# Optimization experiments

Hardware: AMD Instinct MI355X
Metric: run time of the kernel (lower is better)

The kernel has to match this reference:

```python
import jax, jax.numpy as jnp
import numpy as np

D_MODEL = 1024
NUM_HEADS = 16
D_K = D_MODEL // NUM_HEADS


def setup_inputs() -> dict:
    key = jax.random.key(0)
    ks = jax.random.split(key, 12)
    B, S = 2, 2048
    s = 1.0 / np.sqrt(D_MODEL)
    inp = {
        "query": jax.random.normal(ks[0], (B, S, D_MODEL), jnp.float32),
        "key": jax.random.normal(ks[1], (B, S, D_MODEL), jnp.float32),
        "value": jax.random.normal(ks[2], (B, S, D_MODEL), jnp.float32),
        "Wq": jax.random.normal(ks[3], (D_MODEL, D_MODEL), jnp.float32) * s,
        "bq": jax.random.normal(ks[4], (D_MODEL,), jnp.float32) * s,
        "Wk": jax.random.normal(ks[5], (D_MODEL, D_MODEL), jnp.float32) * s,
        "bk": jax.random.normal(ks[6], (D_MODEL,), jnp.float32) * s,
        "Wv": jax.random.normal(ks[7], (D_MODEL, D_MODEL), jnp.float32) * s,
        "bv": jax.random.normal(ks[8], (D_MODEL,), jnp.float32) * s,
        "Wo": jax.random.normal(ks[9], (D_MODEL, D_MODEL), jnp.float32) * s,
        "bo": jax.random.normal(ks[10], (D_MODEL,), jnp.float32) * s,
    }
    return inp


def _split_heads(x):
    B, S, _ = x.shape
    return x.reshape(B, S, NUM_HEADS, D_K).transpose(0, 2, 1, 3)  # [B,H,S,Dk]


def reference(query, key, value, Wq, bq, Wk, bk, Wv, bv, Wo, bo):
    # Linear projections (torch Linear: x @ W.T + b)
    Q = _split_heads(query @ Wq.T + bq)
    K = _split_heads(key @ Wk.T + bk)
    V = _split_heads(value @ Wv.T + bv)
    scale = 1.0 / jnp.sqrt(jnp.asarray(D_K, Q.dtype))
    scores = jnp.einsum('bhqd,bhkd->bhqk', Q, K) * scale  # [B,H,S,S]
    attn = jax.nn.softmax(scores, axis=-1)
    # dropout is identity in eval mode
    x = jnp.einsum('bhqk,bhkd->bhqd', attn, V)
    B, H, S, Dk = x.shape
    x = x.transpose(0, 2, 1, 3).reshape(B, S, H * Dk)
    return x @ Wo.T + bo
```

## Files before the change

### kernel.cpp

```cpp
#include <hip/hip_runtime.h>
#include <hip/hip_bf16.h>

typedef __bf16 bf16;
typedef __attribute__((ext_vector_type(4))) __bf16 bf16x4;
typedef __attribute__((ext_vector_type(8))) __bf16 bf16x8;
typedef __attribute__((ext_vector_type(4))) float f32x4;
typedef __attribute__((ext_vector_type(16))) float f32x16;
typedef unsigned int u32;

#define D_MODEL 1024
#define NHEADS 16
#define DK 64
#define BATCH 2
#define SEQ 2048
#define NTOK (BATCH * SEQ)

#define QSCALE 0.18033688011112042f

__device__ __forceinline__ u32 cvtpk_bf16(float lo, float hi) {
  u32 r;
  asm("v_cvt_pk_bf16_f32 %0, %1, %2" : "=v"(r) : "v"(lo), "v"(hi));
  return r;
}
__device__ __forceinline__ void plswap(u32& a, u32& b) {
  asm("v_permlane32_swap_b32 %0, %1" : "+v"(a), "+v"(b));
}
__device__ __forceinline__ float fast_exp2(float x) {
#if __has_builtin(__builtin_amdgcn_exp2f)
  return __builtin_amdgcn_exp2f(x);
#else
  return exp2f(x);
#endif
}
__device__ __forceinline__ float xhalf_add(float x) {
  return x + __shfl_xor(x, 32);
}

__device__ __forceinline__ int frag_off_q(int s, int d) {
  return ((s >> 5) << 11) + ((d >> 4) << 9) + ((((d >> 3) & 1) * 32 + (s & 31)) << 3) + (d & 7);
}
__device__ __forceinline__ int frag_off_k(int s, int d) {
  return ((s >> 6) << 12) + ((((s >> 5) & 1) * 4 + (d >> 4)) << 9) +
         ((((d >> 3) & 1) * 32 + (s & 31)) << 3) + (d & 7);
}
__device__ __forceinline__ int frag_off_v(int s, int d) {
  return ((s >> 6) << 12) + (((d >> 5) * 4 + ((s >> 4) & 3)) << 9) +
         ((((s >> 3) & 1) * 32 + (d & 31)) << 3) + (s & 7);
}

__global__ __launch_bounds__(256) void cvt3_kernel(
    const float* __restrict__ s0, const float* __restrict__ s1, const float* __restrict__ s2,
    bf16* __restrict__ d0, bf16* __restrict__ d1, bf16* __restrict__ d2, int n4) {
  int i = blockIdx.x * blockDim.x + threadIdx.x;
  if (i >= n4) return;
  const float* s = blockIdx.y == 0 ? s0 : blockIdx.y == 1 ? s1 : s2;
  bf16* d = blockIdx.y == 0 ? d0 : blockIdx.y == 1 ? d1 : d2;
  float4 v = reinterpret_cast<const float4*>(s)[i];
  bf16x4 o;
  o[0] = (bf16)v.x; o[1] = (bf16)v.y; o[2] = (bf16)v.z; o[3] = (bf16)v.w;
  reinterpret_cast<bf16x4*>(d)[i] = o;
}

__global__ __launch_bounds__(256) void cvt4_kernel(
    const float* __restrict__ s0, const float* __restrict__ s1,
    const float* __restrict__ s2, const float* __restrict__ s3,
    bf16* __restrict__ d0, bf16* __restrict__ d1, bf16* __restrict__ d2, bf16* __restrict__ d3,
    int n4) {
  int i = blockIdx.x * blockDim.x + threadIdx.x;
  if (i >= n4) return;
  const float* s = blockIdx.y == 0 ? s0 : blockIdx.y == 1 ? s1 : blockIdx.y == 2 ? s2 : s3;
  bf16* d = blockIdx.y == 0 ? d0 : blockIdx.y == 1 ? d1 : blockIdx.y == 2 ? d2 : d3;
  float4 v = reinterpret_cast<const float4*>(s)[i];
  bf16x4 o;
  o[0] = (bf16)v.x; o[1] = (bf16)v.y; o[2] = (bf16)v.z; o[3] = (bf16)v.w;
  reinterpret_cast<bf16x4*>(d)[i] = o;
}

#define ASYNC_COPY16(gptr, lptr)                                                \
  __builtin_amdgcn_global_load_lds(                                             \
      (__attribute__((address_space(1))) void*)(gptr),                          \
      (__attribute__((address_space(3))) void*)(lptr), 16, 0, 0)

#define BK 32
#define NSTEP (D_MODEL / BK)

struct ProjArgs {
  const bf16* A[3];
  const bf16* W[3];
  const float* bias[3];
  bf16* out[3];
};

__global__ __launch_bounds__(256) void gemm_proj(ProjArgs pa, int K) {
  __shared__ bf16 smem[2][2][128][BK];
  const int z = blockIdx.z;
  const bf16* A = pa.A[z];
  const bf16* Bw = pa.W[z];
  const int m0 = blockIdx.x * 128;
  const int n0 = blockIdx.y * 128;

  const int t = threadIdx.x;
  const int wave = t >> 6;
  const int lane = t & 63;
  const int wr = (wave >> 1) * 64;
  const int wc = (wave & 1) * 64;
  const int r4 = lane >> 2;
  const int c8 = (lane & 3) * 8;
  const int fr = lane & 15;
  const int fk = (lane >> 4) * 8;

  f32x4 acc[4][4] = {};

#define STAGE_PROJ(buf, kk0)                                                    \
  {                                                                             \
    ASYNC_COPY16(&A[(size_t)(m0 + wave * 16 + r4) * K + (kk0) + c8],            \
                 &smem[buf][0][wave * 16][0]);                                  \
    ASYNC_COPY16(&A[(size_t)(m0 + 64 + wave * 16 + r4) * K + (kk0) + c8],       \
                 &smem[buf][0][64 + wave * 16][0]);                             \
    ASYNC_COPY16(&Bw[(size_t)(n0 + wave * 16 + r4) * K + (kk0) + c8],           \
                 &smem[buf][1][wave * 16][0]);                                  \
    ASYNC_COPY16(&Bw[(size_t)(n0 + 64 + wave * 16 + r4) * K + (kk0) + c8],      \
                 &smem[buf][1][64 + wave * 16][0]);                             \
  }

  STAGE_PROJ(0, 0)
  __syncthreads();

  int cur = 0;
  for (int s = 0; s < NSTEP; s++) {
    if (s + 1 < NSTEP) STAGE_PROJ(cur ^ 1, (s + 1) * BK)

    bf16x8 af[4], bfr[4];
#pragma unroll
    for (int m = 0; m < 4; m++)
      af[m] = *reinterpret_cast<const bf16x8*>(&smem[cur][0][wr + m * 16 + fr][fk]);
#pragma unroll
    for (int n = 0; n < 4; n++)
      bfr[n] = *reinterpret_cast<const bf16x8*>(&smem[cur][1][wc + n * 16 + fr][fk]);
#pragma unroll
    for (int m = 0; m < 4; m++)
#pragma unroll
      for (int n = 0; n < 4; n++)
        acc[m][n] = __builtin_amdgcn_mfma_f32_16x16x32_bf16(af[m], bfr[n], acc[m][n], 0, 0, 0);

    __syncthreads();
    cur ^= 1;
  }

  bf16* cbuf = &smem[0][0][0][0];
  const float scale = (z == 0) ? QSCALE : 1.0f;
  const float* bias = pa.bias[z];
#pragma unroll
  for (int m = 0; m < 4; m++) {
#pragma unroll
    for (int n = 0; n < 4; n++) {
      const int col = n0 + wc + n * 16 + fr;
      const float bv = bias[col];
      const int d = col & (DK - 1);
      const int h_loc = (col >> 6) & 1;
#pragma unroll
      for (int j = 0; j < 4; j++) {
        const int rl = wr + m * 16 + (lane >> 4) * 4 + j;
        const float v = (acc[m][n][j] + bv) * scale;
        int inner;
        if (z == 0)      inner = frag_off_q(rl, d);
        else if (z == 1) inner = frag_off_k(rl, d);
        else             inner = frag_off_v(rl, d);
        cbuf[h_loc * 8192 + inner] = (bf16)v;
      }
    }
  }
  __syncthreads();

  {
    const int bblk = m0 >> 11;
    const int ms = m0 & (SEQ - 1);
    const int h_loc = t >> 7;
    const int tl = t & 127;
    const int h = (n0 >> 6) + h_loc;
    bf16* outp = pa.out[z] + ((size_t)(bblk * NHEADS + h)) * SEQ * DK + (size_t)ms * 64;
#pragma unroll
    for (int c = 0; c < 8; c++) {
      const int off_e = (tl + c * 128) * 8;
      *reinterpret_cast<bf16x8*>(&outp[off_e]) =
          *reinterpret_cast<const bf16x8*>(&cbuf[h_loc * 8192 + off_e]);
    }
  }
}

__global__ __launch_bounds__(256) void gemm_out(
    const bf16* __restrict__ A, const bf16* __restrict__ Bw,
    const float* __restrict__ bias, float* __restrict__ out, int K) {
  __shared__ bf16 AsO[2][128][BK];
  __shared__ bf16 BsO[2][64][BK];
  const int m0 = blockIdx.x * 128;
  const int n0 = blockIdx.y * 64;

  const int t = threadIdx.x;
  const int wave = t >> 6;
  const int lane = t & 63;
  const int wr = (wave >> 1) * 64;
  const int wc = (wave & 1) * 32;
  const int r4 = lane >> 2;
  const int c8 = (lane & 3) * 8;
  const int fr = lane & 15;
  const int fk = (lane >> 4) * 8;

  f32x4 acc[4][2] = {};

#define STAGE_OUT(buf, kk0)                                                     \
  {                                                                             \
    ASYNC_COPY16(&A[(size_t)(m0 + wave * 16 + r4) * K + (kk0) + c8],            \
                 &AsO[buf][wave * 16][0]);                                      \
    ASYNC_COPY16(&A[(size_t)(m0 + 64 + wave * 16 + r4) * K + (kk0) + c8],       \
                 &AsO[buf][64 + wave * 16][0]);                                 \
    ASYNC_COPY16(&Bw[(size_t)(n0 + wave * 16 + r4) * K + (kk0) + c8],           \
                 &BsO[buf][wave * 16][0]);                                      \
  }

  STAGE_OUT(0, 0)
  __syncthreads();

  int cur = 0;
  for (int s = 0; s < NSTEP; s++) {
    if (s + 1 < NSTEP) STAGE_OUT(cur ^ 1, (s + 1) * BK)

    bf16x8 af[4], bfr[2];
#pragma unroll
    for (int m = 0; m < 4; m++)
      af[m] = *reinterpret_cast<const bf16x8*>(&AsO[cur][wr + m * 16 + fr][fk]);
#pragma unroll
    for (int n = 0; n < 2; n++)
      bfr[n] = *reinterpret_cast<const bf16x8*>(&BsO[cur][wc + n * 16 + fr][fk]);
#pragma unroll
    for (int m = 0; m < 4; m++)
#pragma unroll
      for (int n = 0; n < 2; n++)
        acc[m][n] = __builtin_amdgcn_mfma_f32_16x16x32_bf16(af[m], bfr[n], acc[m][n], 0, 0, 0);

    __syncthreads();
    cur ^= 1;
  }

#pragma unroll
  for (int m = 0; m < 4; m++) {
#pragma unroll
    for (int n = 0; n < 2; n++) {
      const int col = n0 + wc + n * 16 + fr;
      const float bv = bias[col];
#pragma unroll
      for (int j = 0; j < 4; j++) {
        const int row = m0 + wr + m * 16 + (lane >> 4) * 4 + j;
        out[(size_t)row * D_MODEL + col] = acc[m][n][j] + bv;
      }
    }
  }
}

#define QBLK 32
#define KVBLK 32
#define NT (SEQ / KVBLK)

__global__ __launch_bounds__(256, 2) void attn_kernel(
    const bf16* __restrict__ Qf,
    const bf16* __restrict__ Kf,
    const bf16* __restrict__ Vf,
    bf16* __restrict__ X) {
  const int lane = threadIdx.x & 63;
  const int wave = threadIdx.x >> 6;

  const int i = blockIdx.x;
  const int xcd = i & 7;
  const int slot = i >> 3;
  const int hgrp = slot >> 4;
  const int xq = slot & 15;
  const int bh = xcd + 8 * hgrp;
  const int bb = bh >> 4, hh = bh & (NHEADS - 1);
  const int q0 = xq * (QBLK * 4) + wave * QBLK;
  const int row = lane & 31, hi = lane >> 5;

  const bf16* Qp = Qf + (size_t)bh * SEQ * DK + (size_t)q0 * DK;
  const bf16* Kp = Kf + (size_t)bh * SEQ * DK;
  const bf16* Vp = Vf + (size_t)bh * SEQ * DK;

  bf16x8 qf[4];
#pragma unroll
  for (int kd = 0; kd < 4; kd++)
    qf[kd] = *reinterpret_cast<const bf16x8*>(&Qp[kd * 512 + lane * 8]);

  f32x16 ot0, ot1, fz;
#pragma unroll
  for (int r = 0; r < 16; r++) { ot0[r] = 0.f; ot1[r] = 0.f; fz[r] = 0.f; }
  float l_run = 0.f;

  bf16x8 ka[4], kb[4];

#define LOADK32(dst, tt)                                                        \
  {                                                                             \
    const bf16* kbase_ = Kp + (size_t)(tt) * 2048 + lane * 8;                   \
    _Pragma("unroll") for (int kd = 0; kd < 4; kd++)                            \
        dst[kd] = *reinterpret_cast<const bf16x8*>(&kbase_[kd * 512]);          \
  }

  LOADK32(ka, 0)
  LOADK32(kb, 1)
  f32x16 sa, sb;
  __builtin_amdgcn_s_setprio(1);
  sa = __builtin_amdgcn_mfma_f32_32x32x16_bf16(ka[0], qf[0], fz, 0, 0, 0);
#pragma unroll
  for (int kd = 1; kd < 4; kd++)
    sa = __builtin_amdgcn_mfma_f32_32x32x16_bf16(ka[kd], qf[kd], sa, 0, 0, 0);
  __builtin_amdgcn_s_setprio(0);

  auto pipe = [&](f32x16& SC, f32x16& SN, bf16x8 (&KN)[4], bf16x8 (&KL)[4], int tc) {
    __builtin_amdgcn_s_setprio(1);
    SN = __builtin_amdgcn_mfma_f32_32x32x16_bf16(KN[0], qf[0], fz, 0, 0, 0);
#pragma unroll
    for (int kd = 1; kd < 4; kd++)
      SN = __builtin_amdgcn_mfma_f32_32x32x16_bf16(KN[kd], qf[kd], SN, 0, 0, 0);
    __builtin_amdgcn_s_setprio(0);

    LOADK32(KL, (tc + 2) & (NT - 1))

    bf16x8 vf[2][2];
    {
      const bf16* vbase_ = Vp + (size_t)(tc >> 1) * 4096 + lane * 8;
      const int so = (tc & 1) * 2;
#pragma unroll
      for (int dh = 0; dh < 2; dh++)
#pragma unroll
        for (int ks = 0; ks < 2; ks++)
          vf[dh][ks] = *reinterpret_cast<const bf16x8*>(
              &vbase_[(dh * 4 + so + ks) * 512]);
    }

    float p[16];
#pragma unroll
    for (int r = 0; r < 16; r++) p[r] = fast_exp2(SC[r]);
    float a8[8];
#pragma unroll
    for (int r = 0; r < 8; r++) a8[r] = p[r] + p[r + 8];
#pragma unroll
    for (int r = 0; r < 4; r++) a8[r] += a8[r + 4];
    l_run += (a8[0] + a8[1]) + (a8[2] + a8[3]);

    u32 c[8];
#pragma unroll
    for (int i2 = 0; i2 < 8; i2++) c[i2] = cvtpk_bf16(p[2 * i2], p[2 * i2 + 1]);
    plswap(c[0], c[2]);   plswap(c[1], c[3]);
    plswap(c[4], c[6]);   plswap(c[5], c[7]);
    bf16x8 pbv[2];
#pragma unroll
    for (int ks = 0; ks < 2; ks++) {
      union { u32 u[4]; bf16x8 v; } pk;
      pk.u[0] = c[ks * 4 + 0]; pk.u[1] = c[ks * 4 + 1];
      pk.u[2] = c[ks * 4 + 2]; pk.u[3] = c[ks * 4 + 3];
      pbv[ks] = pk.v;
    }

    __builtin_amdgcn_s_setprio(1);
    ot0 = __builtin_amdgcn_mfma_f32_32x32x16_bf16(vf[0][0], pbv[0], ot0, 0, 0, 0);
    ot0 = __builtin_amdgcn_mfma_f32_32x32x16_bf16(vf[0][1], pbv[1], ot0, 0, 0, 0);
    ot1 = __builtin_amdgcn_mfma_f32_32x32x16_bf16(vf[1][0], pbv[0], ot1, 0, 0, 0);
    ot1 = __builtin_amdgcn_mfma_f32_32x32x16_bf16(vf[1][1], pbv[1], ot1, 0, 0, 0);
    __builtin_amdgcn_s_setprio(0);
  };

  for (int t = 0; t < NT; t += 2) {
    pipe(sa, sb, kb, ka, t);
    pipe(sb, sa, ka, kb, t + 1);
  }

  l_run = xhalf_add(l_run);

  const float inv = 1.0f / l_run;
  bf16* Xp = X + ((size_t)bb * SEQ + q0 + row) * D_MODEL + hh * DK;
#pragma unroll
  for (int g = 0; g < 4; g++) {
    bf16x4 w0, w1;
#pragma unroll
    for (int j = 0; j < 4; j++) {
      w0[j] = (bf16)(ot0[g * 4 + j] * inv);
      w1[j] = (bf16)(ot1[g * 4 + j] * inv);
    }
    *reinterpret_cast<bf16x4*>(&Xp[g * 8 + hi * 4]) = w0;
    *reinterpret_cast<bf16x4*>(&Xp[32 + g * 8 + hi * 4]) = w1;
  }
}

extern "C" void kernel_launch(void* const* d_in, const int* in_sizes, int n_in,
                              void* d_out, int out_size, void* d_ws, size_t ws_size,
                              hipStream_t stream) {
  const float* q  = (const float*)d_in[0];
  const float* k  = (const float*)d_in[1];
  const float* v  = (const float*)d_in[2];
  const float* Wq = (const float*)d_in[3];
  const float* bq = (const float*)d_in[4];
  const float* Wk = (const float*)d_in[5];
  const float* bk = (const float*)d_in[6];
  const float* Wv = (const float*)d_in[7];
  const float* bv = (const float*)d_in[8];
  const float* Wo = (const float*)d_in[9];
  const float* bo = (const float*)d_in[10];

  char* ws = (char*)d_ws;
  size_t off = 0;
  auto alloc = [&](size_t bytes) -> void* {
    void* p = ws + off;
    off += (bytes + 255) & ~(size_t)255;
    return p;
  };
  const size_t ACT = (size_t)NTOK * D_MODEL;
  const size_t WEL = (size_t)D_MODEL * D_MODEL;

  bf16* Xq  = (bf16*)alloc(ACT * 2);
  bf16* Xk  = (bf16*)alloc(ACT * 2);
  bf16* Xv  = (bf16*)alloc(ACT * 2);
  bf16* Wqb = (bf16*)alloc(WEL * 2);
  bf16* Wkb = (bf16*)alloc(WEL * 2);
  bf16* Wvb = (bf16*)alloc(WEL * 2);
  bf16* Wob = (bf16*)alloc(WEL * 2);
  bf16* Qfb = (bf16*)alloc(ACT * 2);
  bf16* Kfb = (bf16*)alloc(ACT * 2);
  bf16* Vfb = (bf16*)alloc(ACT * 2);
  bf16* Xa  = (bf16*)alloc(ACT * 2);

  {
    int n4 = (int)(ACT / 4);
    cvt3_kernel<<<dim3((n4 + 255) / 256, 3), dim3(256), 0, stream>>>(q, k, v, Xq, Xk, Xv, n4);
  }
  {
    int n4 = (int)(WEL / 4);
    cvt4_kernel<<<dim3((n4 + 255) / 256, 4), dim3(256), 0, stream>>>(
        Wq, Wk, Wv, Wo, Wqb, Wkb, Wvb, Wob, n4);
  }

  ProjArgs pa;
  pa.A[0] = Xq;  pa.A[1] = Xk;  pa.A[2] = Xv;
  pa.W[0] = Wqb; pa.W[1] = Wkb; pa.W[2] = Wvb;
  pa.bias[0] = bq; pa.bias[1] = bk; pa.bias[2] = bv;
  pa.out[0] = Qfb; pa.out[1] = Kfb; pa.out[2] = Vfb;
  gemm_proj<<<dim3(NTOK / 128, D_MODEL / 128, 3), dim3(256), 0, stream>>>(pa, D_MODEL);

  attn_kernel<<<dim3(512), dim3(256), 0, stream>>>(Qfb, Kfb, Vfb, Xa);

  gemm_out<<<dim3(NTOK / 128, D_MODEL / 64), dim3(256), 0, stream>>>(
      Xa, Wob, bo, (float*)d_out, D_MODEL);
}
```

Before: 125.4 us.

## Triple-buffer GEMM K-loop with prefetch depth two and merge conversion kernels

Both projection and output GEMMs move from double to triple-buffered LDS staging. Tiles are prefetched two steps ahead, and manual vmcnt waits plus a raw barrier replace __syncthreads, so global loads overlap more compute. The two fp32-to-bf16 conversion launches are merged into one kernel with flat indexing, removing one launch. This raises LDS use per block, which may lower occupancy.

Result: faster. 117.6 us, median of 2 (-6.2%).

```diff
diff --git a/kernel.cpp b/kernel.cpp
--- a/kernel.cpp
+++ b/kernel.cpp
@@ -48,32 +48,29 @@
          ((((s >> 3) & 1) * 32 + (d & 31)) << 3) + (s & 7);
 }
 
-__global__ __launch_bounds__(256) void cvt3_kernel(
-    const float* __restrict__ s0, const float* __restrict__ s1, const float* __restrict__ s2,
-    bf16* __restrict__ d0, bf16* __restrict__ d1, bf16* __restrict__ d2, int n4) {
-  int i = blockIdx.x * blockDim.x + threadIdx.x;
-  if (i >= n4) return;
-  const float* s = blockIdx.y == 0 ? s0 : blockIdx.y == 1 ? s1 : s2;
-  bf16* d = blockIdx.y == 0 ? d0 : blockIdx.y == 1 ? d1 : d2;
-  float4 v = reinterpret_cast<const float4*>(s)[i];
+struct CvtArgs {
+  const float* s[7];
+  bf16* d[7];
+};
+
+#define ACT4 (1 << 20)
+#define WEL4 (1 << 18)
+
+__global__ __launch_bounds__(256) void cvt_all(CvtArgs a) {
+  int i = blockIdx.x * 256 + threadIdx.x;
+  int which, off;
+  if (i < 3 * ACT4) {
+    which = i >> 20;
+    off = i & (ACT4 - 1);
+  } else {
+    int j = i - 3 * ACT4;
+    which = 3 + (j >> 18);
+    off = j & (WEL4 - 1);
+  }
+  float4 v = reinterpret_cast<const float4*>(a.s[which])[off];
   bf16x4 o;
   o[0] = (bf16)v.x; o[1] = (bf16)v.y; o[2] = (bf16)v.z; o[3] = (bf16)v.w;
-  reinterpret_cast<bf16x4*>(d)[i] = o;
-}
-
-__global__ __launch_bounds__(256) void cvt4_kernel(
-    const float* __restrict__ s0, const float* __restrict__ s1,
-    const float* __restrict__ s2, const float* __restrict__ s3,
-    bf16* __restrict__ d0, bf16* __restrict__ d1, bf16* __restrict__ d2, bf16* __restrict__ d3,
-    int n4) {
-  int i = blockIdx.x * blockDim.x + threadIdx.x;
-  if (i >= n4) return;
-  const float* s = blockIdx.y == 0 ? s0 : blockIdx.y == 1 ? s1 : blockIdx.y == 2 ? s2 : s3;
-  bf16* d = blockIdx.y == 0 ? d0 : blockIdx.y == 1 ? d1 : blockIdx.y == 2 ? d2 : d3;
-  float4 v = reinterpret_cast<const float4*>(s)[i];
-  bf16x4 o;
-  o[0] = (bf16)v.x; o[1] = (bf16)v.y; o[2] = (bf16)v.z; o[3] = (bf16)v.w;
-  reinterpret_cast<bf16x4*>(d)[i] = o;
+  reinterpret_cast<bf16x4*>(a.d[which])[off] = o;
 }
 
 #define ASYNC_COPY16(gptr, lptr)                                                \
@@ -92,7 +89,7 @@
 };
 
 __global__ __launch_bounds__(256) void gemm_proj(ProjArgs pa, int K) {
-  __shared__ bf16 smem[2][2][128][BK];
+  __shared__ bf16 smem[3 * 8192];
   const int z = blockIdx.z;
   const bf16* A = pa.A[z];
   const bf16* Bw = pa.W[z];
@@ -111,43 +108,54 @@
 
   f32x4 acc[4][4] = {};
 
-#define STAGE_PROJ(buf, kk0)                                                    \
+#define STAGE_PROJ(slot, kk0)                                                   \
   {                                                                             \
+    bf16* ab_ = &smem[(slot) * 8192];                                           \
     ASYNC_COPY16(&A[(size_t)(m0 + wave * 16 + r4) * K + (kk0) + c8],            \
-                 &smem[buf][0][wave * 16][0]);                                  \
+                 &ab_[(wave * 16) * BK]);                                       \
     ASYNC_COPY16(&A[(size_t)(m0 + 64 + wave * 16 + r4) * K + (kk0) + c8],       \
-                 &smem[buf][0][64 + wave * 16][0]);                             \
+                 &ab_[(64 + wave * 16) * BK]);                                  \
     ASYNC_COPY16(&Bw[(size_t)(n0 + wave * 16 + r4) * K + (kk0) + c8],           \
-                 &smem[buf][1][wave * 16][0]);                                  \
+                 &ab_[4096 + (wave * 16) * BK]);                                \
     ASYNC_COPY16(&Bw[(size_t)(n0 + 64 + wave * 16 + r4) * K + (kk0) + c8],      \
-                 &smem[buf][1][64 + wave * 16][0]);                             \
+                 &ab_[4096 + (64 + wave * 16) * BK]);                           \
   }
 
   STAGE_PROJ(0, 0)
-  __syncthreads();
+  STAGE_PROJ(1, BK)
+  asm volatile("s_waitcnt vmcnt(4)" ::: "memory");
+  __builtin_amdgcn_s_barrier();
 
   int cur = 0;
   for (int s = 0; s < NSTEP; s++) {
-    if (s + 1 < NSTEP) STAGE_PROJ(cur ^ 1, (s + 1) * BK)
-
+    if (s + 2 < NSTEP) {
+      int slot2 = cur + 2; if (slot2 >= 3) slot2 -= 3;
+      STAGE_PROJ(slot2, (s + 2) * BK)
+    }
+
+    const bf16* cb = &smem[cur * 8192];
     bf16x8 af[4], bfr[4];
 #pragma unroll
     for (int m = 0; m < 4; m++)
-      af[m] = *reinterpret_cast<const bf16x8*>(&smem[cur][0][wr + m * 16 + fr][fk]);
+      af[m] = *reinterpret_cast<const bf16x8*>(&cb[(wr + m * 16 + fr) * BK + fk]);
 #pragma unroll
     for (int n = 0; n < 4; n++)
-      bfr[n] = *reinterpret_cast<const bf16x8*>(&smem[cur][1][wc + n * 16 + fr][fk]);
+      bfr[n] = *reinterpret_cast<const bf16x8*>(&cb[4096 + (wc + n * 16 + fr) * BK + fk]);
 #pragma unroll
     for (int m = 0; m < 4; m++)
 #pragma unroll
       for (int n = 0; n < 4; n++)
         acc[m][n] = __builtin_amdgcn_mfma_f32_16x16x32_bf16(af[m], bfr[n], acc[m][n], 0, 0, 0);
 
-    __syncthreads();
-    cur ^= 1;
-  }
-
-  bf16* cbuf = &smem[0][0][0][0];
+    if (s + 2 < NSTEP)
+      asm volatile("s_waitcnt vmcnt(4)" ::: "memory");
+    else
+      asm volatile("s_waitcnt vmcnt(0)" ::: "memory");
+    __builtin_amdgcn_s_barrier();
+    cur = (cur == 2) ? 0 : cur + 1;
+  }
+
+  bf16* cbuf = &smem[0];
   const float scale = (z == 0) ? QSCALE : 1.0f;
   const float* bias = pa.bias[z];
 #pragma unroll
@@ -191,8 +199,7 @@
 __global__ __launch_bounds__(256) void gemm_out(
     const bf16* __restrict__ A, const bf16* __restrict__ Bw,
     const float* __restrict__ bias, float* __restrict__ out, int K) {
-  __shared__ bf16 AsO[2][128][BK];
-  __shared__ bf16 BsO[2][64][BK];
+  __shared__ bf16 smem[3 * 6144];
   const int m0 = blockIdx.x * 128;
   const int n0 = blockIdx.y * 64;
 
@@ -208,38 +215,49 @@
 
   f32x4 acc[4][2] = {};
 
-#define STAGE_OUT(buf, kk0)                                                     \
+#define STAGE_OUT(slot, kk0)                                                    \
   {                                                                             \
+    bf16* ab_ = &smem[(slot) * 6144];                                           \
     ASYNC_COPY16(&A[(size_t)(m0 + wave * 16 + r4) * K + (kk0) + c8],            \
-                 &AsO[buf][wave * 16][0]);                                      \
+                 &ab_[(wave * 16) * BK]);                                       \
     ASYNC_COPY16(&A[(size_t)(m0 + 64 + wave * 16 + r4) * K + (kk0) + c8],       \
-                 &AsO[buf][64 + wave * 16][0]);                                 \
+                 &ab_[(64 + wave * 16) * BK]);                                  \
     ASYNC_COPY16(&Bw[(size_t)(n0 + wave * 16 + r4) * K + (kk0) + c8],           \
-                 &BsO[buf][wave * 16][0]);                                      \
+                 &ab_[4096 + (wave * 16) * BK]);                                \
   }
 
   STAGE_OUT(0, 0)
-  __syncthreads();
+  STAGE_OUT(1, BK)
+  asm volatile("s_waitcnt vmcnt(3)" ::: "memory");
+  __builtin_amdgcn_s_barrier();
 
   int cur = 0;
   for (int s = 0; s < NSTEP; s++) {
-    if (s + 1 < NSTEP) STAGE_OUT(cur ^ 1, (s + 1) * BK)
-
+    if (s + 2 < NSTEP) {
+      int slot2 = cur + 2; if (slot2 >= 3) slot2 -= 3;
+      STAGE_OUT(slot2, (s + 2) * BK)
+    }
+
+    const bf16* cb = &smem[cur * 6144];
     bf16x8 af[4], bfr[2];
 #pragma unroll
     for (int m = 0; m < 4; m++)
-      af[m] = *reinterpret_cast<const bf16x8*>(&AsO[cur][wr + m * 16 + fr][fk]);
+      af[m] = *reinterpret_cast<const bf16x8*>(&cb[(wr + m * 16 + fr) * BK + fk]);
 #pragma unroll
     for (int n = 0; n < 2; n++)
-      bfr[n] = *reinterpret_cast<const bf16x8*>(&BsO[cur][wc + n * 16 + fr][fk]);
+      bfr[n] = *reinterpret_cast<const bf16x8*>(&cb[4096 + (wc + n * 16 + fr) * BK + fk]);
 #pragma unroll
     for (int m = 0; m < 4; m++)
 #pragma unroll
       for (int n = 0; n < 2; n++)
         acc[m][n] = __builtin_amdgcn_mfma_f32_16x16x32_bf16(af[m], bfr[n], acc[m][n], 0, 0, 0);
 
-    __syncthreads();
-    cur ^= 1;
+    if (s + 2 < NSTEP)
+      asm volatile("s_waitcnt vmcnt(3)" ::: "memory");
+    else
+      asm volatile("s_waitcnt vmcnt(0)" ::: "memory");
+    __builtin_amdgcn_s_barrier();
+    cur = (cur == 2) ? 0 : cur + 1;
   }
 
 #pragma unroll
@@ -426,13 +444,13 @@
   bf16* Xa  = (bf16*)alloc(ACT * 2);
 
   {
-    int n4 = (int)(ACT / 4);
-    cvt3_kernel<<<dim3((n4 + 255) / 256, 3), dim3(256), 0, stream>>>(q, k, v, Xq, Xk, Xv, n4);
-  }
-  {
-    int n4 = (int)(WEL / 4);
-    cvt4_kernel<<<dim3((n4 + 255) / 256, 4), dim3(256), 0, stream>>>(
-        Wq, Wk, Wv, Wo, Wqb, Wkb, Wvb, Wob, n4);
+    CvtArgs ca;
+    ca.s[0] = q;  ca.s[1] = k;  ca.s[2] = v;
+    ca.s[3] = Wq; ca.s[4] = Wk; ca.s[5] = Wv; ca.s[6] = Wo;
+    ca.d[0] = Xq;  ca.d[1] = Xk;  ca.d[2] = Xv;
+    ca.d[3] = Wqb; ca.d[4] = Wkb; ca.d[5] = Wvb; ca.d[6] = Wob;
+    const int total = 3 * ACT4 + 4 * WEL4;
+    cvt_all<<<dim3(total / 256), dim3(256), 0, stream>>>(ca);
   }
 
   ProjArgs pa;
```
